# Kernel tuning notes

Hardware: AMD Instinct MI355X
Metric: run time of the kernel (lower is better)

## Reference

```python
import jax, jax.numpy as jnp
import numpy as np

L0 = L1 = L2 = 32          # multiplicities of 0e, 1o, 2o irreps
DIM = L0 + 3 * L1 + 5 * L2  # 288 flat feature dim
N_RBF = 8                   # radial basis size
HID = 64                    # radial MLP hidden
N_PATHS = 7                 # tensor-product paths
CUTOFF = 5.0
AVG_DEG = 16.0


def split_irreps(x):
    x0 = x[:, :L0]                                   # [N, L0]
    x1 = x[:, L0:L0 + 3 * L1].reshape(-1, L1, 3)      # [N, L1, 3]
    x2 = x[:, L0 + 3 * L1:].reshape(-1, L2, 5)        # [N, L2, 5]
    return x0, x1, x2


def merge_irreps(x0, x1, x2):
    n = x0.shape[0]
    return jnp.concatenate([x0, x1.reshape(n, -1), x2.reshape(n, -1)], axis=-1)


def irreps_linear(x, W0, W1, W2):
    # equivariant o3.Linear: per-l channel mixing, shared over m components
    x0, x1, x2 = split_irreps(x)
    y0 = x0 @ W0
    y1 = jnp.einsum('nic,ij->njc', x1, W1)
    y2 = jnp.einsum('nic,ij->njc', x2, W2)
    return merge_irreps(y0, y1, y2)


def sph_harm(u):
    # real spherical harmonics of unit vectors, l=1 and l=2
    x, y, z = u[:, 0], u[:, 1], u[:, 2]
    Y1 = u
    Y2 = jnp.stack([x * y, y * z, (3.0 * z * z - 1.0) / (2.0 * jnp.sqrt(3.0)),
                    x * z, (x * x - y * y) / 2.0], axis=-1)
    return Y1, Y2


def convolution(x, pos, edge_index, Wr1, br1, Wr2):
    # gather neighbor features -> tensor product with Y(r) weighted by radial MLP -> scatter sum
    src, dst = edge_index[0], edge_index[1]
    r = pos[src] - pos[dst]                              # [E, 3]
    d = jnp.sqrt(jnp.sum(r * r, axis=-1) + 1e-12)        # [E]
    u = r / d[:, None]
    Y1, Y2 = sph_harm(u)
    centers = jnp.linspace(0.0, CUTOFF, N_RBF)
    rbf = jnp.exp(-(d[:, None] - centers) ** 2)          # [E, N_RBF]
    h = jax.nn.silu(rbf @ Wr1 + br1)                     # [E, HID]
    w = (h @ Wr2).reshape(-1, N_PATHS, L0)               # [E, 7, mul]

    x0, x1, x2 = split_irreps(x)
    x0s, x1s, x2s = x0[src], x1[src], x2[src]
    # paths: 0:0e*Y0->0e  1:1o*Y0->1o  2:2o*Y0->2o  3:0e*Y1->1o  4:1o*Y1->0e  5:0e*Y2->2o  6:2o*Y2->0e
    m0 = (w[:, 0] * x0s
          + w[:, 4] * jnp.einsum('emc,ec->em', x1s, Y1)
          + w[:, 6] * jnp.einsum('emc,ec->em', x2s, Y2))
    m1 = w[:, 1][:, :, None] * x1s + w[:, 3][:, :, None] * (x0s[:, :, None] * Y1[:, None, :])
    m2 = w[:, 2][:, :, None] * x2s + w[:, 5][:, :, None] * (x0s[:, :, None] * Y2[:, None, :])

    n = x.shape[0]
    norm = 1.0 / np.sqrt(AVG_DEG)
    o0 = jax.ops.segment_sum(m0, dst, num_segments=n) * norm
    o1 = jax.ops.segment_sum(m1, dst, num_segments=n) * norm
    o2 = jax.ops.segment_sum(m2, dst, num_segments=n) * norm
    return merge_irreps(o0, o1, o2)


def gate(x, Wg):
    # NonLinearGate: silu on scalars, sigmoid gates (from scalars) scale l>0 features
    x0, x1, x2 = split_irreps(x)
    g = jax.nn.sigmoid(x0 @ Wg)                          # [N, L1+L2]
    return merge_irreps(jax.nn.silu(x0), x1 * g[:, :L1, None], x2 * g[:, L1:, None])


def setup_inputs() -> dict:
    key = jax.random.key(0)
    ks = jax.random.split(key, 12)
    N, E = 50000, 800000
    nodes = jax.random.normal(ks[0], (N, DIM), dtype=jnp.float32)
    pos = jax.random.uniform(ks[1], (N, 3), dtype=jnp.float32) * 10.0
    batch = jnp.zeros((N,), dtype=jnp.int64)
    edge_index = jax.random.randint(ks[2], (2, E), 0, N, dtype=jnp.int64)
    W0 = jax.random.normal(ks[3], (L0, L0), dtype=jnp.float32) / np.sqrt(L0)
    W1 = jax.random.normal(ks[4], (L1, L1), dtype=jnp.float32) / np.sqrt(L1)
    W2 = jax.random.normal(ks[5], (L2, L2), dtype=jnp.float32) / np.sqrt(L2)
    Wr1 = jax.random.normal(ks[6], (N_RBF, HID), dtype=jnp.float32) / np.sqrt(N_RBF)
    br1 = jnp.zeros((HID,), dtype=jnp.float32)
    Wr2 = jax.random.normal(ks[7], (HID, N_PATHS * L0), dtype=jnp.float32) / np.sqrt(HID)
    Wg = jax.random.normal(ks[8], (L0, L1 + L2), dtype=jnp.float32) / np.sqrt(L0)
    return {"nodes": nodes, "pos": pos, "W0": W0, "W1": W1, "W2": W2,
            "Wr1": Wr1, "br1": br1, "Wr2": Wr2, "Wg": Wg,
            "batch": batch, "edge_index": edge_index}


def reference(nodes, pos, W0, W1, W2, Wr1, br1, Wr2, Wg, batch, edge_index):
    si1 = irreps_linear(nodes, W0, W1, W2)               # owninteraction (shared weights)
    conv = convolution(si1, pos, edge_index, Wr1, br1, Wr2)
    si2 = irreps_linear(conv, W0, W1, W2)                # owninteraction again (same weights)
    mixed = nodes + si2                                  # residual
    return gate(mixed, Wg)
```

## Files before the change

kernel.cpp:

```cpp
#include <hip/hip_runtime.h>
#include <hip/hip_bf16.h>

#define NN 50000
#define NE 800000
#define DIMX 288

typedef float float4v __attribute__((ext_vector_type(4)));
typedef short short8 __attribute__((ext_vector_type(8)));

__device__ __forceinline__ float b2f(unsigned short u) {
  return __uint_as_float(((unsigned int)u) << 16);
}
__device__ __forceinline__ float b2f_lo(unsigned int u) {
  return __uint_as_float(u << 16);
}
__device__ __forceinline__ float b2f_hi(unsigned int u) {
  return __uint_as_float(u & 0xffff0000u);
}
__device__ __forceinline__ unsigned short f2b(float f) {
  unsigned int x = __float_as_uint(f);
  x += 0x7fffu + ((x >> 16) & 1u);
  return (unsigned short)(x >> 16);
}
__device__ __forceinline__ float ldf(const void* p, long i, int f32) {
  return f32 ? ((const float*)p)[i] : b2f(((const unsigned short*)p)[i]);
}
__device__ __forceinline__ int ldidx(const int* p, long i, int i64) {
  return i64 ? p[2 * i] : p[i];
}

__global__ void k_detect(const unsigned short* __restrict__ pos_u16,
                         const int* __restrict__ eidx_i32,
                         int* __restrict__ flags) {
  if (threadIdx.x == 0 && blockIdx.x == 0) {
    int insane = 0;
    for (int i = 0; i < 128; ++i) {
      unsigned short u = pos_u16[i];
      int e = (u >> 7) & 0xff;
      if (e >= 0xC2) insane++;
    }
    flags[0] = (insane >= 2) ? 1 : 0;
    int nz = 0;
    for (int i = 1; i < 16; i += 2) nz += (eidx_i32[i] != 0);
    flags[1] = (nz == 0) ? 1 : 0;
  }
}

__global__ __launch_bounds__(256) void k_prep(
    const void* __restrict__ W0, const void* __restrict__ W1,
    const void* __restrict__ W2, const void* __restrict__ Wg,
    const void* __restrict__ Wr2,
    unsigned short* __restrict__ wr2p,
    unsigned short* __restrict__ w012p,
    unsigned short* __restrict__ wgp,
    int* __restrict__ cnt,
    const int* __restrict__ flags) {
  const int f32 = flags[0];
  int i = blockIdx.x * 256 + threadIdx.x;
  if (i < NN) cnt[i] = 0;
  if (blockIdx.x != 0) return;
  for (int idx = threadIdx.x; idx < 28 * 512; idx += 256) {
    int f = idx >> 9, r = idx & 511;
    int lane = r >> 3, ii = r & 7;
    int q = lane >> 4, colA = lane & 15;
    int t = f >> 1, hf = f & 1;
    int k = hf * 32 + q * 8 + ii;
    int j = t * 16 + colA;
    wr2p[idx] = f2b(ldf(Wr2, (long)k * 224 + j, f32));
  }
  for (int idx = threadIdx.x; idx < 6 * 512; idx += 256) {
    int f = idx >> 9, r = idx & 511;
    int lane = r >> 3, ii = r & 7;
    int q = lane >> 4, colA = lane & 15;
    int w = f >> 1, t = f & 1;
    const void* W = (w == 0) ? W0 : ((w == 1) ? W1 : W2);
    w012p[idx] = f2b(ldf(W, (long)(q * 8 + ii) * 32 + t * 16 + colA, f32));
  }
  for (int idx = threadIdx.x; idx < 4 * 512; idx += 256) {
    int t = idx >> 9, r = idx & 511;
    int lane = r >> 3, ii = r & 7;
    int q = lane >> 4, colA = lane & 15;
    wgp[idx] = f2b(ldf(Wg, (long)(q * 8 + ii) * 64 + t * 16 + colA, f32));
  }
}

__global__ __launch_bounds__(256) void k_hist(const int* __restrict__ eidx,
                                              int* __restrict__ cnt,
                                              const int* __restrict__ flags) {
  const int i64 = flags[1];
  long e = (long)blockIdx.x * 256 + threadIdx.x;
  if (e < NE) {
    int d = ldidx(eidx, NE + e, i64);
    atomicAdd(&cnt[d], 1);
  }
}

__global__ __launch_bounds__(256) void k_scan1(const int* __restrict__ cnt,
                                               int* __restrict__ bsum) {
  __shared__ int part[256];
  int t = threadIdx.x;
  int i = blockIdx.x * 256 + t;
  part[t] = (i < NN) ? cnt[i] : 0;
  __syncthreads();
  for (int off = 128; off > 0; off >>= 1) {
    if (t < off) part[t] += part[t + off];
    __syncthreads();
  }
  if (t == 0) bsum[blockIdx.x] = part[0];
}

__global__ __launch_bounds__(256) void k_scan2(const int* __restrict__ bsum,
                                               int* __restrict__ boff) {
  __shared__ int part[256];
  int t = threadIdx.x;
  int v = (t < 196) ? bsum[t] : 0;
  part[t] = v;
  __syncthreads();
  for (int off = 1; off < 256; off <<= 1) {
    int u = (t >= off) ? part[t - off] : 0;
    __syncthreads();
    part[t] += u;
    __syncthreads();
  }
  if (t < 196) boff[t] = part[t] - v;
}

__global__ __launch_bounds__(256) void k_scan3(const int* __restrict__ cnt,
                                               const int* __restrict__ boff,
                                               int* __restrict__ cursor) {
  __shared__ int part[256];
  int t = threadIdx.x;
  int i = blockIdx.x * 256 + t;
  int v = (i < NN) ? cnt[i] : 0;
  part[t] = v;
  __syncthreads();
  for (int off = 1; off < 256; off <<= 1) {
    int u = (t >= off) ? part[t - off] : 0;
    __syncthreads();
    part[t] += u;
    __syncthreads();
  }
  if (i < NN) cursor[i] = boff[blockIdx.x] + part[t] - v;
}

__global__ __launch_bounds__(256) void k_scatter(const int* __restrict__ eidx,
                                                 int* __restrict__ cursor,
                                                 unsigned long long* __restrict__ sedge,
                                                 const int* __restrict__ flags) {
  const int i64 = flags[1];
  long e = (long)blockIdx.x * 256 + threadIdx.x;
  if (e < NE) {
    int s = ldidx(eidx, e, i64);
    int d = ldidx(eidx, NE + e, i64);
    int p = atomicAdd(&cursor[d], 1);
    sedge[p] = ((unsigned long long)(unsigned)d << 32) | (unsigned)s;
  }
}

__global__ __launch_bounds__(256) void k_linear1(
    const void* __restrict__ nodes,
    const unsigned short* __restrict__ w012p,
    unsigned short* __restrict__ si1,
    float* __restrict__ conv,
    const int* __restrict__ flags) {
  const int f32 = flags[0];
  __shared__ __align__(16) unsigned short wf[3072];
  __shared__ __align__(16) unsigned int xs32[64 * 145];
  int tid = threadIdx.x, lane = tid & 63, wid = tid >> 6;
  for (int idx = tid; idx < 384; idx += 256)
    ((uint4*)wf)[idx] = ((const uint4*)w012p)[idx];
  long nbase = (long)blockIdx.x * 64;
  for (int idx = tid; idx < 64 * 144; idx += 256) {
    int row = idx / 144, cp = idx - row * 144;
    long rowg = nbase + row; if (rowg >= NN) rowg = NN - 1;
    unsigned v;
    if (f32) {
      const float* rp = (const float*)nodes + rowg * DIMX + 2 * cp;
      v = ((unsigned)f2b(rp[1]) << 16) | f2b(rp[0]);
    } else {
      v = ((const unsigned*)nodes)[rowg * 144 + cp];
    }
    xs32[row * 145 + cp] = v;
  }
  {
    float4 z; z.x = 0.f; z.y = 0.f; z.z = 0.f; z.w = 0.f;
    long start = nbase * DIMX / 4;
    long end = start + 64 * DIMX / 4;
    long lim = (long)NN * DIMX / 4;
    if (end > lim) end = lim;
    float4* cz = (float4*)conv;
    for (long idx = start + tid; idx < end; idx += 256) cz[idx] = z;
  }
  __syncthreads();
  long tbase = nbase + (long)wid * 16;
  if (tbase >= NN) return;
  const int q = lane >> 4, colA = lane & 15;
  const unsigned short* xs16 = (const unsigned short*)xs32;
  const int rb = (wid * 16 + colA) * 290;
  short8 a0f, a1f0, a1f1, a1f2, a2f0, a2f1, a2f2, a2f3, a2f4;
  #pragma unroll
  for (int i = 0; i < 8; ++i) {
    int k = q * 8 + i;
    a0f[i]  = (short)xs16[rb + k];
    a1f0[i] = (short)xs16[rb + 32 + 3 * k + 0];
    a1f1[i] = (short)xs16[rb + 32 + 3 * k + 1];
    a1f2[i] = (short)xs16[rb + 32 + 3 * k + 2];
    a2f0[i] = (short)xs16[rb + 128 + 5 * k + 0];
    a2f1[i] = (short)xs16[rb + 128 + 5 * k + 1];
    a2f2[i] = (short)xs16[rb + 128 + 5 * k + 2];
    a2f3[i] = (short)xs16[rb + 128 + 5 * k + 3];
    a2f4[i] = (short)xs16[rb + 128 + 5 * k + 4];
  }
  const short8* wv = (const short8*)wf;
  float4v zf = {0.f, 0.f, 0.f, 0.f};
  float4v D0[2], D1[3][2], D2[5][2];
  #pragma unroll
  for (int t = 0; t < 2; ++t) {
    D0[t]    = __builtin_amdgcn_mfma_f32_16x16x32_bf16(a0f,  wv[(0 + t) * 64 + lane], zf, 0, 0, 0);
    D1[0][t] = __builtin_amdgcn_mfma_f32_16x16x32_bf16(a1f0, wv[(2 + t) * 64 + lane], zf, 0, 0, 0);
    D1[1][t] = __builtin_amdgcn_mfma_f32_16x16x32_bf16(a1f1, wv[(2 + t) * 64 + lane], zf, 0, 0, 0);
    D1[2][t] = __builtin_amdgcn_mfma_f32_16x16x32_bf16(a1f2, wv[(2 + t) * 64 + lane], zf, 0, 0, 0);
    D2[0][t] = __builtin_amdgcn_mfma_f32_16x16x32_bf16(a2f0, wv[(4 + t) * 64 + lane], zf, 0, 0, 0);
    D2[1][t] = __builtin_amdgcn_mfma_f32_16x16x32_bf16(a2f1, wv[(4 + t) * 64 + lane], zf, 0, 0, 0);
    D2[2][t] = __builtin_amdgcn_mfma_f32_16x16x32_bf16(a2f2, wv[(4 + t) * 64 + lane], zf, 0, 0, 0);
    D2[3][t] = __builtin_amdgcn_mfma_f32_16x16x32_bf16(a2f3, wv[(4 + t) * 64 + lane], zf, 0, 0, 0);
    D2[4][t] = __builtin_amdgcn_mfma_f32_16x16x32_bf16(a2f4, wv[(4 + t) * 64 + lane], zf, 0, 0, 0);
  }
  #pragma unroll
  for (int t = 0; t < 2; ++t) {
    #pragma unroll
    for (int r = 0; r < 4; ++r) {
      long node = tbase + q * 4 + r;
      if (node < NN) {
        int mj = t * 16 + colA;
        unsigned short* row = si1 + (size_t)node * DIMX;
        short8 pk;
        pk[0] = (short)f2b(D0[t][r]);
        pk[1] = (short)f2b(D1[0][t][r]);
        pk[2] = (short)f2b(D1[1][t][r]);
        pk[3] = (short)f2b(D1[2][t][r]);
        pk[4] = (short)f2b(D2[0][t][r]);
        pk[5] = (short)f2b(D2[1][t][r]);
        pk[6] = (short)f2b(D2[2][t][r]);
        pk[7] = (short)f2b(D2[3][t][r]);
        *(short8*)(row + mj * 8) = pk;
        row[256 + mj] = f2b(D2[4][t][r]);
      }
    }
  }
}

__device__ __forceinline__ void flushrow(float* __restrict__ conv, unsigned dstn,
                                         float accv[9], int h, int o0, int o1, int o2,
                                         bool at) {
  float tot[9];
  #pragma unroll
  for (int r = 0; r < 9; ++r) tot[r] = accv[r] + __shfl_xor(accv[r], 32, 64);
  float* cv = conv + (size_t)dstn * DIMX;
  if (at) {
    if (h == 0) {
      atomicAdd(cv + o0, tot[0]);
      atomicAdd(cv + o1, tot[1]); atomicAdd(cv + o1 + 1, tot[2]); atomicAdd(cv + o1 + 2, tot[3]);
      atomicAdd(cv + o2, tot[4]);
    } else {
      atomicAdd(cv + o2 + 1, tot[5]); atomicAdd(cv + o2 + 2, tot[6]);
      atomicAdd(cv + o2 + 3, tot[7]); atomicAdd(cv + o2 + 4, tot[8]);
    }
  } else {
    if (h == 0) {
      cv[o0] = tot[0];
      cv[o1] = tot[1]; cv[o1 + 1] = tot[2]; cv[o1 + 2] = tot[3];
      cv[o2] = tot[4];
    } else {
      cv[o2 + 1] = tot[5]; cv[o2 + 2] = tot[6];
      cv[o2 + 3] = tot[7]; cv[o2 + 4] = tot[8];
    }
  }
  #pragma unroll
  for (int r = 0; r < 9; ++r) accv[r] = 0.f;
}

__global__ __launch_bounds__(256) void k_edges(
    const void* __restrict__ pos,
    const unsigned long long* __restrict__ sedge,
    const void* __restrict__ Wr1,
    const void* __restrict__ br1,
    const unsigned short* __restrict__ wr2p,
    const unsigned short* __restrict__ si1,
    float* __restrict__ conv,
    const int* __restrict__ flags) {
  const int f32 = flags[0];
  __shared__ __align__(16) unsigned short wr2t[14336];
  __shared__ __align__(16) unsigned short wall[4][4032];
  __shared__ __align__(16) float wr1s[576];
  __shared__ __align__(16) float geomW[4][16][8];
  __shared__ __align__(16) float rbfW[4][16][8];
  __shared__ unsigned int sdvR[4][2][2][16];
  int tid = threadIdx.x, lane = tid & 63, wid = tid >> 6;

  for (int idx = tid; idx < 1792; idx += 256)
    ((uint4*)wr2t)[idx] = ((const uint4*)wr2p)[idx];
  for (int idx = tid; idx < 512; idx += 256) wr1s[idx] = ldf(Wr1, idx, f32);
  if (tid < 64) wr1s[512 + tid] = ldf(br1, tid, f32);
  __syncthreads();

  size_t we = (size_t)blockIdx.x * 512 + (size_t)wid * 128;
  if (we >= (size_t)NE) return;

  const int q = lane >> 4, colA = lane & 15;
  const int h = lane >> 5, m = lane & 31;
  const int o0 = m, o1 = 32 + 3 * m, o2 = 128 + 5 * m;
  unsigned short* WL = wall[wid];

  unsigned left_dst = 0xffffffffu, right_dst = 0xffffffffu;
  if (we > 0) left_dst = (unsigned)(sedge[we - 1] >> 32);
  if (we + 128 < (size_t)NE) right_dst = (unsigned)(sedge[we + 128] >> 32);

  if (lane < 16) {
    unsigned long long pr = sedge[we + lane];
    sdvR[wid][0][0][lane] = (unsigned)(pr & 0xffffffffu);
    sdvR[wid][0][1][lane] = (unsigned)(pr >> 32);
  }
  asm volatile("" ::: "memory");

  unsigned cur_d = sdvR[wid][0][1][0];
  bool first = true;
  float accv[9];
  #pragma unroll
  for (int r = 0; r < 9; ++r) accv[r] = 0.f;

  uint4 A0, A1, A2, A3; unsigned short E0, E1, E2, E3;
  {
    const char* rp;
    unsigned s;
    s = sdvR[wid][0][0][0 + h]; rp = (const char*)si1 + (size_t)s * 576;
    A0 = *(const uint4*)(rp + m * 16); E0 = *(const unsigned short*)(rp + 512 + 2 * m);
    s = sdvR[wid][0][0][2 + h]; rp = (const char*)si1 + (size_t)s * 576;
    A1 = *(const uint4*)(rp + m * 16); E1 = *(const unsigned short*)(rp + 512 + 2 * m);
    s = sdvR[wid][0][0][4 + h]; rp = (const char*)si1 + (size_t)s * 576;
    A2 = *(const uint4*)(rp + m * 16); E2 = *(const unsigned short*)(rp + 512 + 2 * m);
    s = sdvR[wid][0][0][6 + h]; rp = (const char*)si1 + (size_t)s * 576;
    A3 = *(const uint4*)(rp + m * 16); E3 = *(const unsigned short*)(rp + 512 + 2 * m);
  }

  #pragma unroll 1
  for (int g = 0; g < 8; ++g) {
    if (lane < 16) {
      if (g < 7) {
        unsigned long long pr = sedge[we + (size_t)(g + 1) * 16 + lane];
        sdvR[wid][(g + 1) & 1][0][lane] = (unsigned)(pr & 0xffffffffu);
        sdvR[wid][(g + 1) & 1][1][lane] = (unsigned)(pr >> 32);
      }
      unsigned s = sdvR[wid][g & 1][0][lane];
      unsigned d = sdvR[wid][g & 1][1][lane];
      float rx = ldf(pos, 3 * (long)s, f32)     - ldf(pos, 3 * (long)d, f32);
      float ry = ldf(pos, 3 * (long)s + 1, f32) - ldf(pos, 3 * (long)d + 1, f32);
      float rz = ldf(pos, 3 * (long)s + 2, f32) - ldf(pos, 3 * (long)d + 2, f32);
      float dd = sqrtf(rx * rx + ry * ry + rz * rz + 1e-12f);
      float inv = 1.0f / dd;
      float ux = rx * inv, uy = ry * inv, uz = rz * inv;
      geomW[wid][lane][0] = ux; geomW[wid][lane][1] = uy; geomW[wid][lane][2] = uz;
      geomW[wid][lane][3] = ux * uy;
      geomW[wid][lane][4] = uy * uz;
      geomW[wid][lane][5] = (3.f * uz * uz - 1.f) * 0.28867513459481287f;
      geomW[wid][lane][6] = ux * uz;
      geomW[wid][lane][7] = (ux * ux - uy * uy) * 0.5f;
      #pragma unroll
      for (int k = 0; k < 8; ++k) {
        float t = dd - (float)k * (5.0f / 7.0f);
        rbfW[wid][lane][k] = __expf(-t * t);
      }
    }
    asm volatile("" ::: "memory");

    short8 afrag0, afrag1;
    {
      const float* rb = &rbfW[wid][colA][0];
      float rbv[8];
      #pragma unroll
      for (int r = 0; r < 8; ++r) rbv[r] = rb[r];
      float a0[8], a1[8];
      {
        float4v b0 = *(const float4v*)&wr1s[512 + q * 8];
        float4v b1 = *(const float4v*)&wr1s[512 + q * 8 + 4];
        float4v b2 = *(const float4v*)&wr1s[512 + 32 + q * 8];
        float4v b3 = *(const float4v*)&wr1s[512 + 32 + q * 8 + 4];
        #pragma unroll
        for (int i = 0; i < 4; ++i) {
          a0[i] = b0[i]; a0[4 + i] = b1[i];
          a1[i] = b2[i]; a1[4 + i] = b3[i];
        }
      }
      #pragma unroll
      for (int r = 0; r < 8; ++r) {
        float4v wA = *(const float4v*)&wr1s[r * 64 + q * 8];
        float4v wB = *(const float4v*)&wr1s[r * 64 + q * 8 + 4];
        float4v wC = *(const float4v*)&wr1s[r * 64 + 32 + q * 8];
        float4v wD = *(const float4v*)&wr1s[r * 64 + 32 + q * 8 + 4];
        float rv = rbv[r];
        #pragma unroll
        for (int i = 0; i < 4; ++i) {
          a0[i]     += rv * wA[i];
          a0[4 + i] += rv * wB[i];
          a1[i]     += rv * wC[i];
          a1[4 + i] += rv * wD[i];
        }
      }
      #pragma unroll
      for (int i = 0; i < 8; ++i) {
        float a = a0[i];
        afrag0[i] = (short)f2b(0.25f * a / (1.f + __expf(-a)));
        float a2 = a1[i];
        afrag1[i] = (short)f2b(0.25f * a2 / (1.f + __expf(-a2)));
      }
    }

    {
      float4v acc[14];
      #pragma unroll
      for (int t = 0; t < 14; ++t) {
        short8 b0 = *(const short8*)&wr2t[(t * 2 + 0) * 512 + lane * 8];
        short8 b1 = *(const short8*)&wr2t[(t * 2 + 1) * 512 + lane * 8];
        float4v c = {0.f, 0.f, 0.f, 0.f};
        c = __builtin_amdgcn_mfma_f32_16x16x32_bf16(afrag0, b0, c, 0, 0, 0);
        c = __builtin_amdgcn_mfma_f32_16x16x32_bf16(afrag1, b1, c, 0, 0, 0);
        acc[t] = c;
      }
      #pragma unroll
      for (int t = 0; t < 14; ++t) {
        int j = t * 16 + colA;
        #pragma unroll
        for (int r = 0; r < 4; ++r)
          WL[j * 18 + q * 4 + r] = f2b(acc[t][r]);
      }
    }
    asm volatile("" ::: "memory");

    #pragma unroll
    for (int ii = 0; ii < 8; ++ii) {
      uint4 cur; unsigned short ce;
      switch (ii & 3) {
        case 0: cur = A0; ce = E0; break;
        case 1: cur = A1; ce = E1; break;
        case 2: cur = A2; ce = E2; break;
        default: cur = A3; ce = E3; break;
      }
      if (!(g == 7 && ii >= 4)) {
        int adv = 2 * ii + 8 + h;
        int pslot = (g + (adv >> 4)) & 1;
        int pidx = adv & 15;
        unsigned ps = sdvR[wid][pslot][0][pidx];
        const char* rp = (const char*)si1 + (size_t)ps * 576;
        uint4 pa = *(const uint4*)(rp + m * 16);
        unsigned short pe = *(const unsigned short*)(rp + 512 + 2 * m);
        switch (ii & 3) {
          case 0: A0 = pa; E0 = pe; break;
          case 1: A1 = pa; E1 = pe; break;
          case 2: A2 = pa; E2 = pe; break;
          default: A3 = pa; E3 = pe; break;
        }
      }

      unsigned dn0 = sdvR[wid][g & 1][1][2 * ii];
      unsigned dn1 = sdvR[wid][g & 1][1][2 * ii + 1];

      if (dn0 != cur_d) {
        bool at = first && (cur_d == left_dst);
        flushrow(conv, cur_d, accv, h, o0, o1, o2, at);
        first = false;
        cur_d = dn0;
      }

      float x0v = b2f_lo(cur.x), x1a = b2f_hi(cur.x);
      float x1b = b2f_lo(cur.y), x1c = b2f_hi(cur.y);
      float x2a = b2f_lo(cur.z), x2b = b2f_hi(cur.z);
      float x2c = b2f_lo(cur.w), x2d = b2f_hi(cur.w);
      float x2e = b2f(ce);
      const int elc = 2 * ii + h;
      float w0 = b2f(WL[(0 * 32 + m) * 18 + elc]);
      float w1 = b2f(WL[(1 * 32 + m) * 18 + elc]);
      float w2 = b2f(WL[(2 * 32 + m) * 18 + elc]);
      float w3 = b2f(WL[(3 * 32 + m) * 18 + elc]);
      float w4 = b2f(WL[(4 * 32 + m) * 18 + elc]);
      float w5 = b2f(WL[(5 * 32 + m) * 18 + elc]);
      float w6 = b2f(WL[(6 * 32 + m) * 18 + elc]);
      float4v gv0 = *(const float4v*)&geomW[wid][elc][0];
      float4v gv1 = *(const float4v*)&geomW[wid][elc][4];
      float y1x = gv0[0], y1y = gv0[1], y1z = gv0[2], y20 = gv0[3];
      float y21 = gv1[0], y22 = gv1[1], y23 = gv1[2], y24 = gv1[3];
      float d1 = x1a * y1x + x1b * y1y + x1c * y1z;
      float d2 = x2a * y20 + x2b * y21 + x2c * y22 + x2d * y23 + x2e * y24;
      float w3x0 = w3 * x0v, w5x0 = w5 * x0v;
      float v[9];
      v[0] = w0 * x0v + w4 * d1 + w6 * d2;
      v[1] = w1 * x1a + w3x0 * y1x;
      v[2] = w1 * x1b + w3x0 * y1y;
      v[3] = w1 * x1c + w3x0 * y1z;
      v[4] = w2 * x2a + w5x0 * y20;
      v[5] = w2 * x2b + w5x0 * y21;
      v[6] = w2 * x2c + w5x0 * y22;
      v[7] = w2 * x2d + w5x0 * y23;
      v[8] = w2 * x2e + w5x0 * y24;

      if (dn1 == dn0) {
        #pragma unroll
        for (int r = 0; r < 9; ++r) accv[r] += v[r];
      } else {
        if (h == 0) {
          #pragma unroll
          for (int r = 0; r < 9; ++r) accv[r] += v[r];
        }
        bool at = first && (cur_d == left_dst);
        flushrow(conv, cur_d, accv, h, o0, o1, o2, at);
        first = false;
        cur_d = dn1;
        if (h == 1) {
          #pragma unroll
          for (int r = 0; r < 9; ++r) accv[r] += v[r];
        }
      }
    }
  }
  {
    bool at = (cur_d == right_dst) || (first && (cur_d == left_dst));
    flushrow(conv, cur_d, accv, h, o0, o1, o2, at);
  }
}

__global__ __launch_bounds__(256) void k_gate(
    const float* __restrict__ conv,
    const void* __restrict__ nodes,
    const unsigned short* __restrict__ w012p,
    const unsigned short* __restrict__ wgp,
    float* __restrict__ out,
    const int* __restrict__ flags) {
  const int f32 = flags[0];
  __shared__ __align__(16) unsigned short wf[5120];
  __shared__ __align__(16) unsigned int xs32[64 * 145];
  __shared__ unsigned short m0b[4][16][40];
  __shared__ float gsb[4][16][66];
  int tid = threadIdx.x, lane = tid & 63, wid = tid >> 6;
  for (int idx = tid; idx < 384; idx += 256)
    ((uint4*)wf)[idx] = ((const uint4*)w012p)[idx];
  for (int idx = tid; idx < 256; idx += 256)
    ((uint4*)(wf + 3072))[idx] = ((const uint4*)wgp)[idx];
  long nbase = (long)blockIdx.x * 64;
  for (int idx = tid; idx < 64 * 144; idx += 256) {
    int row = idx / 144, cp = idx - row * 144;
    long rowg = nbase + row; if (rowg >= NN) rowg = NN - 1;
    const float* rp = conv + rowg * DIMX + 2 * cp;
    xs32[row * 145 + cp] = ((unsigned)f2b(rp[1]) << 16) | f2b(rp[0]);
  }
  __syncthreads();
  long tbase = nbase + (long)wid * 16;
  if (tbase >= NN) return;
  const int q = lane >> 4, colA = lane & 15;
  const unsigned short* xs16 = (const unsigned short*)xs32;
  const int rb = (wid * 16 + colA) * 290;
  short8 a0f, a1f0, a1f1, a1f2, a2f0, a2f1, a2f2, a2f3, a2f4;
  #pragma unroll
  for (int i = 0; i < 8; ++i) {
    int k = q * 8 + i;
    a0f[i]  = (short)xs16[rb + k];
    a1f0[i] = (short)xs16[rb + 32 + 3 * k + 0];
    a1f1[i] = (short)xs16[rb + 32 + 3 * k + 1];
    a1f2[i] = (short)xs16[rb + 32 + 3 * k + 2];
    a2f0[i] = (short)xs16[rb + 128 + 5 * k + 0];
    a2f1[i] = (short)xs16[rb + 128 + 5 * k + 1];
    a2f2[i] = (short)xs16[rb + 128 + 5 * k + 2];
    a2f3[i] = (short)xs16[rb + 128 + 5 * k + 3];
    a2f4[i] = (short)xs16[rb + 128 + 5 * k + 4];
  }
  const short8* wv = (const short8*)wf;
  const short8* wg = (const short8*)(wf + 3072);
  float4v zf = {0.f, 0.f, 0.f, 0.f};
  float mixed0[2][4];
  #pragma unroll
  for (int t = 0; t < 2; ++t) {
    float4v d = __builtin_amdgcn_mfma_f32_16x16x32_bf16(a0f, wv[(0 + t) * 64 + lane], zf, 0, 0, 0);
    #pragma unroll
    for (int r = 0; r < 4; ++r) {
      long node = tbase + q * 4 + r;
      long nc = node < NN ? node : NN - 1;
      float v = d[r] + ldf(nodes, nc * DIMX + t * 16 + colA, f32);
      mixed0[t][r] = v;
      m0b[wid][q * 4 + r][t * 16 + colA] = f2b(v);
    }
  }
  asm volatile("" ::: "memory");
  short8 amf;
  #pragma unroll
  for (int i = 0; i < 8; ++i) amf[i] = (short)m0b[wid][colA][q * 8 + i];
  #pragma unroll
  for (int t = 0; t < 4; ++t) {
    float4v d = __builtin_amdgcn_mfma_f32_16x16x32_bf16(amf, wg[t * 64 + lane], zf, 0, 0, 0);
    #pragma unroll
    for (int r = 0; r < 4; ++r)
      gsb[wid][q * 4 + r][t * 16 + colA] = 1.f / (1.f + __expf(-d[r]));
  }
  asm volatile("" ::: "memory");
  float4v D1[3][2], D2[5][2];
  #pragma unroll
  for (int t = 0; t < 2; ++t) {
    D1[0][t] = __builtin_amdgcn_mfma_f32_16x16x32_bf16(a1f0, wv[(2 + t) * 64 + lane], zf, 0, 0, 0);
    D1[1][t] = __builtin_amdgcn_mfma_f32_16x16x32_bf16(a1f1, wv[(2 + t) * 64 + lane], zf, 0, 0, 0);
    D1[2][t] = __builtin_amdgcn_mfma_f32_16x16x32_bf16(a1f2, wv[(2 + t) * 64 + lane], zf, 0, 0, 0);
    D2[0][t] = __builtin_amdgcn_mfma_f32_16x16x32_bf16(a2f0, wv[(4 + t) * 64 + lane], zf, 0, 0, 0);
    D2[1][t] = __builtin_amdgcn_mfma_f32_16x16x32_bf16(a2f1, wv[(4 + t) * 64 + lane], zf, 0, 0, 0);
    D2[2][t] = __builtin_amdgcn_mfma_f32_16x16x32_bf16(a2f2, wv[(4 + t) * 64 + lane], zf, 0, 0, 0);
    D2[3][t] = __builtin_amdgcn_mfma_f32_16x16x32_bf16(a2f3, wv[(4 + t) * 64 + lane], zf, 0, 0, 0);
    D2[4][t] = __builtin_amdgcn_mfma_f32_16x16x32_bf16(a2f4, wv[(4 + t) * 64 + lane], zf, 0, 0, 0);
  }
  #pragma unroll
  for (int t = 0; t < 2; ++t) {
    #pragma unroll
    for (int r = 0; r < 4; ++r) {
      long node = tbase + q * 4 + r;
      if (node < NN) {
        int nl = q * 4 + r;
        int mj = t * 16 + colA;
        float* orow = out + (size_t)node * DIMX;
        const long nrow = node * DIMX;
        float v0 = mixed0[t][r];
        orow[mj] = v0 / (1.f + __expf(-v0));
        float g1 = gsb[wid][nl][mj];
        float g2 = gsb[wid][nl][32 + mj];
        #pragma unroll
        for (int c = 0; c < 3; ++c) {
          float v = D1[c][t][r] + ldf(nodes, nrow + 32 + 3 * mj + c, f32);
          orow[32 + 3 * mj + c] = v * g1;
        }
        #pragma unroll
        for (int c = 0; c < 5; ++c) {
          float v = D2[c][t][r] + ldf(nodes, nrow + 128 + 5 * mj + c, f32);
          orow[128 + 5 * mj + c] = v * g2;
        }
      }
    }
  }
}

extern "C" void kernel_launch(void* const* d_in, const int* in_sizes, int n_in,
                              void* d_out, int out_size, void* d_ws, size_t ws_size,
                              hipStream_t stream) {
  const void* nodes = d_in[0];
  const void* pos   = d_in[1];
  const void* W0    = d_in[2];
  const void* W1    = d_in[3];
  const void* W2    = d_in[4];
  const void* Wr1   = d_in[5];
  const void* br1   = d_in[6];
  const void* Wr2   = d_in[7];
  const void* Wg    = d_in[8];
  const int* eidx   = (const int*)d_in[10];

  int* flags = (int*)d_ws;
  unsigned short* si1 = (unsigned short*)((char*)d_ws + 256);
  size_t conv_off = 256 + (size_t)NN * DIMX * 2;
  float* conv = (float*)((char*)d_ws + conv_off);
  size_t cnt_off = conv_off + (size_t)NN * DIMX * 4;
  int* cnt    = (int*)((char*)d_ws + cnt_off);
  int* cursor = (int*)((char*)d_ws + cnt_off + (size_t)NN * 4);
  unsigned long long* sedge =
      (unsigned long long*)((char*)d_ws + cnt_off + 2 * (size_t)NN * 4);
  unsigned short* wr2p =
      (unsigned short*)((char*)d_ws + cnt_off + 2 * (size_t)NN * 4 + (size_t)NE * 8);
  unsigned short* w012p = wr2p + 28 * 512;
  unsigned short* wgp   = w012p + 6 * 512;
  int* bsum = (int*)(wgp + 4 * 512);
  int* boff = bsum + 256;
  float* out = (float*)d_out;

  hipLaunchKernelGGL(k_detect, dim3(1), dim3(64), 0, stream,
                     (const unsigned short*)pos, eidx, flags);
  hipLaunchKernelGGL(k_prep, dim3((NN + 255) / 256), dim3(256), 0, stream,
                     W0, W1, W2, Wg, Wr2, wr2p, w012p, wgp, cnt, flags);
  hipLaunchKernelGGL(k_hist, dim3((NE + 255) / 256), dim3(256), 0, stream, eidx, cnt, flags);
  hipLaunchKernelGGL(k_scan1, dim3((NN + 255) / 256), dim3(256), 0, stream, cnt, bsum);
  hipLaunchKernelGGL(k_scan2, dim3(1), dim3(256), 0, stream, bsum, boff);
  hipLaunchKernelGGL(k_scan3, dim3((NN + 255) / 256), dim3(256), 0, stream, cnt, boff, cursor);
  hipLaunchKernelGGL(k_scatter, dim3((NE + 255) / 256), dim3(256), 0, stream,
                     eidx, cursor, sedge, flags);
  hipLaunchKernelGGL(k_linear1, dim3((NN + 63) / 64), dim3(256), 0, stream,
                     nodes, w012p, si1, conv, flags);
  hipLaunchKernelGGL(k_edges, dim3((NE + 511) / 512), dim3(256), 0, stream,
                     pos, sedge, Wr1, br1, wr2p, si1, conv, flags);
  hipLaunchKernelGGL(k_gate, dim3((NN + 63) / 64), dim3(256), 0, stream,
                     conv, nodes, w012p, wgp, out, flags);
}
```

Measured before the change: 564.4 us.

## Deepen edge gather prefetch, vectorize radial weight LDS reads, fold detect into prep

The edge kernel now prefetches source-node rows a full 16-edge group ahead using eight register buffers instead of four, which should hide more global gather latency. The per-edge radial weights are stored in LDS in a transposed layout with the seven path weights contiguous, so one 16-byte load replaces seven scalar LDS reads. The separate dtype-detection kernel is merged into the prep kernel to remove one launch. The costs are more registers per thread, which may lower occupancy, and a slightly larger shared-memory buffer.

```diff
diff --git a/kernel.cpp b/kernel.cpp
--- a/kernel.cpp
+++ b/kernel.cpp
@@ -29,36 +29,37 @@
   return i64 ? p[2 * i] : p[i];
 }
 
-__global__ void k_detect(const unsigned short* __restrict__ pos_u16,
-                         const int* __restrict__ eidx_i32,
-                         int* __restrict__ flags) {
-  if (threadIdx.x == 0 && blockIdx.x == 0) {
-    int insane = 0;
-    for (int i = 0; i < 128; ++i) {
-      unsigned short u = pos_u16[i];
-      int e = (u >> 7) & 0xff;
-      if (e >= 0xC2) insane++;
-    }
-    flags[0] = (insane >= 2) ? 1 : 0;
-    int nz = 0;
-    for (int i = 1; i < 16; i += 2) nz += (eidx_i32[i] != 0);
-    flags[1] = (nz == 0) ? 1 : 0;
-  }
-}
-
 __global__ __launch_bounds__(256) void k_prep(
     const void* __restrict__ W0, const void* __restrict__ W1,
     const void* __restrict__ W2, const void* __restrict__ Wg,
     const void* __restrict__ Wr2,
+    const unsigned short* __restrict__ pos_u16,
+    const int* __restrict__ eidx_i32,
     unsigned short* __restrict__ wr2p,
     unsigned short* __restrict__ w012p,
     unsigned short* __restrict__ wgp,
     int* __restrict__ cnt,
-    const int* __restrict__ flags) {
-  const int f32 = flags[0];
+    int* __restrict__ flags) {
   int i = blockIdx.x * 256 + threadIdx.x;
   if (i < NN) cnt[i] = 0;
   if (blockIdx.x != 0) return;
+  __shared__ int lf;
+  if (threadIdx.x == 0) {
+    int insane = 0;
+    for (int k = 0; k < 128; ++k) {
+      unsigned short u = pos_u16[k];
+      int e = (u >> 7) & 0xff;
+      if (e >= 0xC2) insane++;
+    }
+    int f0 = (insane >= 2) ? 1 : 0;
+    int nz = 0;
+    for (int k = 1; k < 16; k += 2) nz += (eidx_i32[k] != 0);
+    flags[0] = f0;
+    flags[1] = (nz == 0) ? 1 : 0;
+    lf = f0;
+  }
+  __syncthreads();
+  const int f32 = lf;
   for (int idx = threadIdx.x; idx < 28 * 512; idx += 256) {
     int f = idx >> 9, r = idx & 511;
     int lane = r >> 3, ii = r & 7;
@@ -291,7 +292,7 @@
     const int* __restrict__ flags) {
   const int f32 = flags[0];
   __shared__ __align__(16) unsigned short wr2t[14336];
-  __shared__ __align__(16) unsigned short wall[4][4032];
+  __shared__ __align__(16) unsigned short wall[4][4352];
   __shared__ __align__(16) float wr1s[576];
   __shared__ __align__(16) float geomW[4][16][8];
   __shared__ __align__(16) float rbfW[4][16][8];
@@ -329,18 +330,27 @@
   #pragma unroll
   for (int r = 0; r < 9; ++r) accv[r] = 0.f;
 
-  uint4 A0, A1, A2, A3; unsigned short E0, E1, E2, E3;
+  uint4 A0, A1, A2, A3, A4, A5, A6, A7;
+  unsigned short E0, E1, E2, E3, E4, E5, E6, E7;
   {
     const char* rp;
     unsigned s;
-    s = sdvR[wid][0][0][0 + h]; rp = (const char*)si1 + (size_t)s * 576;
+    s = sdvR[wid][0][0][0 + h];  rp = (const char*)si1 + (size_t)s * 576;
     A0 = *(const uint4*)(rp + m * 16); E0 = *(const unsigned short*)(rp + 512 + 2 * m);
-    s = sdvR[wid][0][0][2 + h]; rp = (const char*)si1 + (size_t)s * 576;
+    s = sdvR[wid][0][0][2 + h];  rp = (const char*)si1 + (size_t)s * 576;
     A1 = *(const uint4*)(rp + m * 16); E1 = *(const unsigned short*)(rp + 512 + 2 * m);
-    s = sdvR[wid][0][0][4 + h]; rp = (const char*)si1 + (size_t)s * 576;
+    s = sdvR[wid][0][0][4 + h];  rp = (const char*)si1 + (size_t)s * 576;
     A2 = *(const uint4*)(rp + m * 16); E2 = *(const unsigned short*)(rp + 512 + 2 * m);
-    s = sdvR[wid][0][0][6 + h]; rp = (const char*)si1 + (size_t)s * 576;
+    s = sdvR[wid][0][0][6 + h];  rp = (const char*)si1 + (size_t)s * 576;
     A3 = *(const uint4*)(rp + m * 16); E3 = *(const unsigned short*)(rp + 512 + 2 * m);
+    s = sdvR[wid][0][0][8 + h];  rp = (const char*)si1 + (size_t)s * 576;
+    A4 = *(const uint4*)(rp + m * 16); E4 = *(const unsigned short*)(rp + 512 + 2 * m);
+    s = sdvR[wid][0][0][10 + h]; rp = (const char*)si1 + (size_t)s * 576;
+    A5 = *(const uint4*)(rp + m * 16); E5 = *(const unsigned short*)(rp + 512 + 2 * m);
+    s = sdvR[wid][0][0][12 + h]; rp = (const char*)si1 + (size_t)s * 576;
+    A6 = *(const uint4*)(rp + m * 16); E6 = *(const unsigned short*)(rp + 512 + 2 * m);
+    s = sdvR[wid][0][0][14 + h]; rp = (const char*)si1 + (size_t)s * 576;
+    A7 = *(const uint4*)(rp + m * 16); E7 = *(const unsigned short*)(rp + 512 + 2 * m);
   }
 
   #pragma unroll 1
@@ -429,9 +439,10 @@
       #pragma unroll
       for (int t = 0; t < 14; ++t) {
         int j = t * 16 + colA;
+        int mm = j & 31, cc = j >> 5;
         #pragma unroll
         for (int r = 0; r < 4; ++r)
-          WL[j * 18 + q * 4 + r] = f2b(acc[t][r]);
+          WL[mm * 136 + (q * 4 + r) * 8 + cc] = f2b(acc[t][r]);
       }
     }
     asm volatile("" ::: "memory");
@@ -439,25 +450,31 @@
     #pragma unroll
     for (int ii = 0; ii < 8; ++ii) {
       uint4 cur; unsigned short ce;
-      switch (ii & 3) {
+      switch (ii) {
         case 0: cur = A0; ce = E0; break;
         case 1: cur = A1; ce = E1; break;
         case 2: cur = A2; ce = E2; break;
-        default: cur = A3; ce = E3; break;
-      }
-      if (!(g == 7 && ii >= 4)) {
-        int adv = 2 * ii + 8 + h;
-        int pslot = (g + (adv >> 4)) & 1;
-        int pidx = adv & 15;
-        unsigned ps = sdvR[wid][pslot][0][pidx];
+        case 3: cur = A3; ce = E3; break;
+        case 4: cur = A4; ce = E4; break;
+        case 5: cur = A5; ce = E5; break;
+        case 6: cur = A6; ce = E6; break;
+        default: cur = A7; ce = E7; break;
+      }
+      if (g < 7) {
+        int pidx = 2 * ii + h;
+        unsigned ps = sdvR[wid][(g + 1) & 1][0][pidx];
         const char* rp = (const char*)si1 + (size_t)ps * 576;
         uint4 pa = *(const uint4*)(rp + m * 16);
         unsigned short pe = *(const unsigned short*)(rp + 512 + 2 * m);
-        switch (ii & 3) {
+        switch (ii) {
           case 0: A0 = pa; E0 = pe; break;
           case 1: A1 = pa; E1 = pe; break;
           case 2: A2 = pa; E2 = pe; break;
-          default: A3 = pa; E3 = pe; break;
+          case 3: A3 = pa; E3 = pe; break;
+          case 4: A4 = pa; E4 = pe; break;
+          case 5: A5 = pa; E5 = pe; break;
+          case 6: A6 = pa; E6 = pe; break;
+          default: A7 = pa; E7 = pe; break;
         }
       }
 
@@ -477,13 +494,14 @@
       float x2c = b2f_lo(cur.w), x2d = b2f_hi(cur.w);
       float x2e = b2f(ce);
       const int elc = 2 * ii + h;
-      float w0 = b2f(WL[(0 * 32 + m) * 18 + elc]);
-      float w1 = b2f(WL[(1 * 32 + m) * 18 + elc]);
-      float w2 = b2f(WL[(2 * 32 + m) * 18 + elc]);
-      float w3 = b2f(WL[(3 * 32 + m) * 18 + elc]);
-      float w4 = b2f(WL[(4 * 32 + m) * 18 + elc]);
-      float w5 = b2f(WL[(5 * 32 + m) * 18 + elc]);
-      float w6 = b2f(WL[(6 * 32 + m) * 18 + elc]);
+      short8 wv8 = *(const short8*)&WL[m * 136 + elc * 8];
+      float w0 = b2f((unsigned short)wv8[0]);
+      float w1 = b2f((unsigned short)wv8[1]);
+      float w2 = b2f((unsigned short)wv8[2]);
+      float w3 = b2f((unsigned short)wv8[3]);
+      float w4 = b2f((unsigned short)wv8[4]);
+      float w5 = b2f((unsigned short)wv8[5]);
+      float w6 = b2f((unsigned short)wv8[6]);
       float4v gv0 = *(const float4v*)&geomW[wid][elc][0];
       float4v gv1 = *(const float4v*)&geomW[wid][elc][4];
       float y1x = gv0[0], y1y = gv0[1], y1z = gv0[2], y20 = gv0[3];
@@ -671,10 +689,10 @@
   int* boff = bsum + 256;
   float* out = (float*)d_out;
 
-  hipLaunchKernelGGL(k_detect, dim3(1), dim3(64), 0, stream,
-                     (const unsigned short*)pos, eidx, flags);
   hipLaunchKernelGGL(k_prep, dim3((NN + 255) / 256), dim3(256), 0, stream,
-                     W0, W1, W2, Wg, Wr2, wr2p, w012p, wgp, cnt, flags);
+                     W0, W1, W2, Wg, Wr2,
+                     (const unsigned short*)pos, eidx,
+                     wr2p, w012p, wgp, cnt, flags);
   hipLaunchKernelGGL(k_hist, dim3((NE + 255) / 256), dim3(256), 0, stream, eidx, cnt, flags);
   hipLaunchKernelGGL(k_scan1, dim3((NN + 255) / 256), dim3(256), 0, stream, cnt, bsum);
   hipLaunchKernelGGL(k_scan2, dim3(1), dim3(256), 0, stream, bsum, boff);
```

New measurement: 560.3 us. Within noise of the previous version (-0.7%).

## Read radial weights from global in edge kernel, shrink LDS, fold detect into prep

Applied to the files above, without the earlier changes.

The edge kernel stops staging the 28KB packed Wr2 matrix in shared memory and instead loads MFMA B fragments directly from global/L2, with the tile loop split into two non-unrolled halves to limit register pressure. Shared memory usage drops, which allows more blocks per CU. The per-wave weight scratch stride changes from 18 to 17 to reduce LDS bank conflicts. The separate detect kernel is merged into block 0 of the prep kernel, removing one launch. The trade-off is extra global/L2 traffic for B fragments on every tile iteration.

```diff
diff --git a/kernel.cpp b/kernel.cpp
--- a/kernel.cpp
+++ b/kernel.cpp
@@ -29,36 +29,37 @@
   return i64 ? p[2 * i] : p[i];
 }
 
-__global__ void k_detect(const unsigned short* __restrict__ pos_u16,
-                         const int* __restrict__ eidx_i32,
-                         int* __restrict__ flags) {
-  if (threadIdx.x == 0 && blockIdx.x == 0) {
-    int insane = 0;
-    for (int i = 0; i < 128; ++i) {
-      unsigned short u = pos_u16[i];
-      int e = (u >> 7) & 0xff;
-      if (e >= 0xC2) insane++;
-    }
-    flags[0] = (insane >= 2) ? 1 : 0;
-    int nz = 0;
-    for (int i = 1; i < 16; i += 2) nz += (eidx_i32[i] != 0);
-    flags[1] = (nz == 0) ? 1 : 0;
-  }
-}
-
 __global__ __launch_bounds__(256) void k_prep(
     const void* __restrict__ W0, const void* __restrict__ W1,
     const void* __restrict__ W2, const void* __restrict__ Wg,
     const void* __restrict__ Wr2,
+    const unsigned short* __restrict__ pos_u16,
+    const int* __restrict__ eidx_i32,
     unsigned short* __restrict__ wr2p,
     unsigned short* __restrict__ w012p,
     unsigned short* __restrict__ wgp,
     int* __restrict__ cnt,
-    const int* __restrict__ flags) {
-  const int f32 = flags[0];
+    int* __restrict__ flags) {
   int i = blockIdx.x * 256 + threadIdx.x;
   if (i < NN) cnt[i] = 0;
   if (blockIdx.x != 0) return;
+  __shared__ int lf;
+  if (threadIdx.x == 0) {
+    int insane = 0;
+    for (int k = 0; k < 128; ++k) {
+      unsigned short u = pos_u16[k];
+      int e = (u >> 7) & 0xff;
+      if (e >= 0xC2) insane++;
+    }
+    int f0 = (insane >= 2) ? 1 : 0;
+    int nz = 0;
+    for (int k = 1; k < 16; k += 2) nz += (eidx_i32[k] != 0);
+    flags[0] = f0;
+    flags[1] = (nz == 0) ? 1 : 0;
+    lf = f0;
+  }
+  __syncthreads();
+  const int f32 = lf;
   for (int idx = threadIdx.x; idx < 28 * 512; idx += 256) {
     int f = idx >> 9, r = idx & 511;
     int lane = r >> 3, ii = r & 7;
@@ -290,16 +291,13 @@
     float* __restrict__ conv,
     const int* __restrict__ flags) {
   const int f32 = flags[0];
-  __shared__ __align__(16) unsigned short wr2t[14336];
-  __shared__ __align__(16) unsigned short wall[4][4032];
+  __shared__ __align__(16) unsigned short wall[4][3808];
   __shared__ __align__(16) float wr1s[576];
   __shared__ __align__(16) float geomW[4][16][8];
   __shared__ __align__(16) float rbfW[4][16][8];
   __shared__ unsigned int sdvR[4][2][2][16];
   int tid = threadIdx.x, lane = tid & 63, wid = tid >> 6;
 
-  for (int idx = tid; idx < 1792; idx += 256)
-    ((uint4*)wr2t)[idx] = ((const uint4*)wr2p)[idx];
   for (int idx = tid; idx < 512; idx += 256) wr1s[idx] = ldf(Wr1, idx, f32);
   if (tid < 64) wr1s[512 + tid] = ldf(br1, tid, f32);
   __syncthreads();
@@ -311,6 +309,7 @@
   const int h = lane >> 5, m = lane & 31;
   const int o0 = m, o1 = 32 + 3 * m, o2 = 128 + 5 * m;
   unsigned short* WL = wall[wid];
+  const short8* wr2f = (const short8*)wr2p;
 
   unsigned left_dst = 0xffffffffu, right_dst = 0xffffffffu;
   if (we > 0) left_dst = (unsigned)(sedge[we - 1] >> 32);
@@ -417,21 +416,25 @@
 
     {
       float4v acc[14];
-      #pragma unroll
-      for (int t = 0; t < 14; ++t) {
-        short8 b0 = *(const short8*)&wr2t[(t * 2 + 0) * 512 + lane * 8];
-        short8 b1 = *(const short8*)&wr2t[(t * 2 + 1) * 512 + lane * 8];
-        float4v c = {0.f, 0.f, 0.f, 0.f};
-        c = __builtin_amdgcn_mfma_f32_16x16x32_bf16(afrag0, b0, c, 0, 0, 0);
-        c = __builtin_amdgcn_mfma_f32_16x16x32_bf16(afrag1, b1, c, 0, 0, 0);
-        acc[t] = c;
+      #pragma unroll 1
+      for (int tc = 0; tc < 2; ++tc) {
+        #pragma unroll
+        for (int t7 = 0; t7 < 7; ++t7) {
+          int t = tc * 7 + t7;
+          short8 b0 = wr2f[(t * 2 + 0) * 64 + lane];
+          short8 b1 = wr2f[(t * 2 + 1) * 64 + lane];
+          float4v c = {0.f, 0.f, 0.f, 0.f};
+          c = __builtin_amdgcn_mfma_f32_16x16x32_bf16(afrag0, b0, c, 0, 0, 0);
+          c = __builtin_amdgcn_mfma_f32_16x16x32_bf16(afrag1, b1, c, 0, 0, 0);
+          acc[t] = c;
+        }
       }
       #pragma unroll
       for (int t = 0; t < 14; ++t) {
         int j = t * 16 + colA;
         #pragma unroll
         for (int r = 0; r < 4; ++r)
-          WL[j * 18 + q * 4 + r] = f2b(acc[t][r]);
+          WL[j * 17 + q * 4 + r] = f2b(acc[t][r]);
       }
     }
     asm volatile("" ::: "memory");
@@ -477,13 +480,13 @@
       float x2c = b2f_lo(cur.w), x2d = b2f_hi(cur.w);
       float x2e = b2f(ce);
       const int elc = 2 * ii + h;
-      float w0 = b2f(WL[(0 * 32 + m) * 18 + elc]);
-      float w1 = b2f(WL[(1 * 32 + m) * 18 + elc]);
-      float w2 = b2f(WL[(2 * 32 + m) * 18 + elc]);
-      float w3 = b2f(WL[(3 * 32 + m) * 18 + elc]);
-      float w4 = b2f(WL[(4 * 32 + m) * 18 + elc]);
-      float w5 = b2f(WL[(5 * 32 + m) * 18 + elc]);
-      float w6 = b2f(WL[(6 * 32 + m) * 18 + elc]);
+      float w0 = b2f(WL[(0 * 32 + m) * 17 + elc]);
+      float w1 = b2f(WL[(1 * 32 + m) * 17 + elc]);
+      float w2 = b2f(WL[(2 * 32 + m) * 17 + elc]);
+      float w3 = b2f(WL[(3 * 32 + m) * 17 + elc]);
+      float w4 = b2f(WL[(4 * 32 + m) * 17 + elc]);
+      float w5 = b2f(WL[(5 * 32 + m) * 17 + elc]);
+      float w6 = b2f(WL[(6 * 32 + m) * 17 + elc]);
       float4v gv0 = *(const float4v*)&geomW[wid][elc][0];
       float4v gv1 = *(const float4v*)&geomW[wid][elc][4];
       float y1x = gv0[0], y1y = gv0[1], y1z = gv0[2], y20 = gv0[3];
@@ -671,10 +674,10 @@
   int* boff = bsum + 256;
   float* out = (float*)d_out;
 
-  hipLaunchKernelGGL(k_detect, dim3(1), dim3(64), 0, stream,
-                     (const unsigned short*)pos, eidx, flags);
   hipLaunchKernelGGL(k_prep, dim3((NN + 255) / 256), dim3(256), 0, stream,
-                     W0, W1, W2, Wg, Wr2, wr2p, w012p, wgp, cnt, flags);
+                     W0, W1, W2, Wg, Wr2,
+                     (const unsigned short*)pos, eidx,
+                     wr2p, w012p, wgp, cnt, flags);
   hipLaunchKernelGGL(k_hist, dim3((NE + 255) / 256), dim3(256), 0, stream, eidx, cnt, flags);
   hipLaunchKernelGGL(k_scan1, dim3((NN + 255) / 256), dim3(256), 0, stream, cnt, bsum);
   hipLaunchKernelGGL(k_scan2, dim3(1), dim3(256), 0, stream, bsum, boff);
```

Measured after the change: 748.2 us. 32.6% more time.
